# Kernel optimization log

Measured on AMD Instinct MI355X. Metric: run time of the kernel, lower is better.

## Reference

```python
import jax, jax.numpy as jnp
import numpy as np

N = 50000      # nodes
E = 800000     # edges (before self-loops)
F_IN = 256
H = 8          # heads layer 1
C = 64         # hidden channels per head
OUT = 40       # classes
NEG_SLOPE = 0.2


def setup_inputs() -> dict:
    key = jax.random.key(0)
    ks = jax.random.split(key, 10)
    sc = 0.05
    return {
        "x": jax.random.normal(ks[0], (N, F_IN), jnp.float32),
        "edge_index": jax.random.randint(ks[1], (2, E), 0, N, dtype=jnp.int64),
        "W1": jax.random.normal(ks[2], (F_IN, H * C), jnp.float32) * sc,
        "a_src1": jax.random.normal(ks[3], (H, C), jnp.float32) * sc,
        "a_dst1": jax.random.normal(ks[4], (H, C), jnp.float32) * sc,
        "b1": jnp.zeros((H * C,), jnp.float32),
        "W2": jax.random.normal(ks[5], (H * C, OUT), jnp.float32) * sc,
        "a_src2": jax.random.normal(ks[6], (1, OUT), jnp.float32) * sc,
        "a_dst2": jax.random.normal(ks[7], (1, OUT), jnp.float32) * sc,
        "b2": jnp.zeros((OUT,), jnp.float32),
    }


def gat_layer(h_in, src, dst, W, a_s, a_d, b, heads, ch, concat, n):
    # h: [n, heads, ch] per-head linear transform
    h = (h_in @ W).reshape(n, heads, ch)
    alpha_s = jnp.sum(h * a_s, axis=-1)   # [n, heads]
    alpha_d = jnp.sum(h * a_d, axis=-1)   # [n, heads]
    # edge-wise raw attention logits [E, heads]
    e = jax.nn.leaky_relu(alpha_s[src] + alpha_d[dst], NEG_SLOPE)
    # segment softmax over incoming edges of each dst node
    m = jax.ops.segment_max(e, dst, num_segments=n)
    w = jnp.exp(e - m[dst])
    s = jax.ops.segment_sum(w, dst, num_segments=n)
    alpha = w / s[dst]                    # [E, heads]
    # scatter-aggregate messages: [n, heads, ch]
    out = jax.ops.segment_sum(h[src] * alpha[:, :, None], dst, num_segments=n)
    out = out.reshape(n, heads * ch) if concat else out.mean(axis=1)
    return out + b


def reference(x, edge_index, W1, a_src1, a_dst1, b1, W2, a_src2, a_dst2, b2):
    # add self-loops (PyG GATConv default); guarantees every dst has >=1 edge
    loop = jnp.arange(N, dtype=edge_index.dtype)
    src = jnp.concatenate([edge_index[0], loop])
    dst = jnp.concatenate([edge_index[1], loop])
    h = gat_layer(x, src, dst, W1, a_src1, a_dst1, b1, H, C, True, N)
    h = jax.nn.relu(h)  # dropout is identity in eval mode
    out = gat_layer(h, src, dst, W2, a_src2, a_dst2, b2, 1, OUT, False, N)
    return jax.nn.log_softmax(out, axis=1)
```

## Files before the change

kernel.cpp:

```cpp
#include <hip/hip_runtime.h>

#define N_NODES 50000
#define N_EDGES 800000
#define F_INK   256
#define HC      512
#define OUT_C   40
#define OUT_P   48
#define NEG     0.2f
#define CAP     64
#define GEMM_NB 782

typedef short short8 __attribute__((ext_vector_type(8)));
typedef float f32x4 __attribute__((ext_vector_type(4)));
typedef float f32x2 __attribute__((ext_vector_type(2)));

__device__ __forceinline__ float bf2f(unsigned short u) {
    union { unsigned int i; float f; } v; v.i = ((unsigned int)u) << 16; return v.f;
}
__device__ __forceinline__ unsigned short f2bf(float f) {
    union { float f; unsigned int i; } v; v.f = f;
    unsigned int x = v.i;
    return (unsigned short)((x + 0x7fffu + ((x >> 16) & 1u)) >> 16);
}
__device__ __forceinline__ float bflo(unsigned int u) {
    union { unsigned int i; float f; } v; v.i = u << 16; return v.f;
}
__device__ __forceinline__ float bfhi(unsigned int u) {
    union { unsigned int i; float f; } v; v.i = u & 0xffff0000u; return v.f;
}
__device__ __forceinline__ bool ei_is64(const int* ei) {
    return ei[1] == 0 && ei[3] == 0 && ei[5] == 0;
}
__device__ __forceinline__ float lrelu(float x) { return x > 0.f ? x : NEG * x; }
__device__ __forceinline__ unsigned char f2fp8(float v) {
    return (unsigned char)(__builtin_amdgcn_cvt_pk_fp8_f32(v, v, 0, false) & 0xff);
}
__device__ __forceinline__ float fp82f(unsigned char b) {
    f32x2 p = __builtin_amdgcn_cvt_pk_f32_fp8((int)b, false);
    return p[0];
}

__global__ __launch_bounds__(256) void prep_k(const float* __restrict__ W1, const float* __restrict__ W2,
                       const float* __restrict__ s1, const float* __restrict__ d1, const float* __restrict__ b1,
                       const float* __restrict__ s2, const float* __restrict__ d2, const float* __restrict__ b2,
                       unsigned short* __restrict__ W1p, unsigned short* __restrict__ W2p,
                       unsigned short* __restrict__ s1c, unsigned short* __restrict__ d1c,
                       unsigned short* __restrict__ b1c, unsigned short* __restrict__ s2c,
                       unsigned short* __restrict__ d2c, unsigned short* __restrict__ b2c,
                       int* __restrict__ cnt, int* __restrict__ srcs) {
    int b = blockIdx.x;
    if (b < 512) {
        int t = b * 256 + threadIdx.x;
        int k = t / HC, n = t % HC;
        int s = k >> 5, q = (k >> 3) & 3, j = k & 7;
        W1p[((((s << 2) + q) * HC + n) << 3) + j] = f2bf(W1[k * HC + n]);
    } else if (b < 608) {
        int t = (b - 512) * 256 + threadIdx.x;
        int k = t / OUT_P, n = t % OUT_P;
        int s = k >> 5, q = (k >> 3) & 3, j = k & 7;
        unsigned short v = (n < OUT_C) ? f2bf(W2[k * OUT_C + n]) : (unsigned short)0;
        W2p[((((s << 2) + q) * OUT_P + n) << 3) + j] = v;
    } else if (b == 608) {
        int t = threadIdx.x;
        for (int j = t; j < 512; j += 256) {
            s1c[j] = f2bf(s1[j]); d1c[j] = f2bf(d1[j]); b1c[j] = f2bf(b1[j]);
        }
        if (t < OUT_C) { s2c[t] = f2bf(s2[t]); d2c[t] = f2bf(d2[t]); b2c[t] = f2bf(b2[t]); }
    } else {
        int i = (b - 609) * 256 + threadIdx.x;
        if (i < N_NODES) {
            cnt[i] = 1;
            srcs[(size_t)i * CAP] = i;
        }
    }
}

__global__ __launch_bounds__(256) void gemm1_k(const float* __restrict__ x,
                                               const unsigned short* __restrict__ Wp,
                                               const unsigned short* __restrict__ a_s,
                                               const unsigned short* __restrict__ a_d,
                                               unsigned char* __restrict__ h1f8,
                                               float* __restrict__ as1, float* __restrict__ ad1,
                                               const int* __restrict__ ei,
                                               int* __restrict__ cnt, int* __restrict__ srcs) {
    __shared__ unsigned short xs[64 * 264];
    int tid = threadIdx.x;
    if (blockIdx.x >= GEMM_NB) {
        int e = (blockIdx.x - GEMM_NB) * 256 + tid;
        if (e < N_EDGES) {
            bool is64 = ei_is64(ei);
            int src = is64 ? ei[2 * e] : ei[e];
            int dst = is64 ? ei[2 * N_EDGES + 2 * e] : ei[N_EDGES + e];
            int pos = atomicAdd(&cnt[dst], 1);
            if (pos < CAP) srcs[(size_t)dst * CAP + pos] = src;
        }
        return;
    }
    int bm = blockIdx.x;
    int row0 = bm * 64;
#pragma unroll
    for (int it = 0; it < 16; it++) {
        int j = tid + it * 256;
        int r = j >> 6;
        int c = (j & 63) << 2;
        int rr = row0 + r; rr = rr < N_NODES ? rr : N_NODES - 1;
        float4 f = *reinterpret_cast<const float4*>(x + (size_t)rr * F_INK + c);
        unsigned int lo = (unsigned int)f2bf(f.x) | ((unsigned int)f2bf(f.y) << 16);
        unsigned int hi = (unsigned int)f2bf(f.z) | ((unsigned int)f2bf(f.w) << 16);
        *reinterpret_cast<uint2*>(&xs[r * 264 + c]) = make_uint2(lo, hi);
    }
    __syncthreads();
    int w = tid >> 6, lane = tid & 63;
    int q = lane >> 4, l16 = lane & 15;
    short8 a[8];
#pragma unroll
    for (int s = 0; s < 8; s++)
        a[s] = *reinterpret_cast<const short8*>(&xs[(w * 16 + l16) * 264 + s * 32 + q * 8]);
    int orow = row0 + w * 16 + q * 4;
#pragma unroll
    for (int bn = 0; bn < 8; bn++) {
        f32x4 acc[4];
#pragma unroll
        for (int t = 0; t < 4; t++) acc[t] = (f32x4){0.f, 0.f, 0.f, 0.f};
#pragma unroll
        for (int s = 0; s < 8; s++) {
#pragma unroll
            for (int t = 0; t < 4; t++) {
                int col = bn * 64 + t * 16 + l16;
                short8 b = *reinterpret_cast<const short8*>(Wp + ((((s << 2) + q) * HC + col) << 3));
                acc[t] = __builtin_amdgcn_mfma_f32_16x16x32_bf16(a[s], b, acc[t], 0, 0, 0);
            }
        }
        float sa0 = 0.f, sa1 = 0.f, sa2 = 0.f, sa3 = 0.f;
        float da0 = 0.f, da1 = 0.f, da2 = 0.f, da3 = 0.f;
#pragma unroll
        for (int t = 0; t < 4; t++) {
            int col = bn * 64 + t * 16 + l16;
            float asc = bf2f(a_s[col]);
            float adc = bf2f(a_d[col]);
            float v0 = acc[t][0], v1 = acc[t][1], v2 = acc[t][2], v3 = acc[t][3];
            sa0 += v0 * asc; da0 += v0 * adc;
            sa1 += v1 * asc; da1 += v1 * adc;
            sa2 += v2 * asc; da2 += v2 * adc;
            sa3 += v3 * asc; da3 += v3 * adc;
            if (orow + 3 < N_NODES) {
                h1f8[(size_t)(orow + 0) * HC + col] = f2fp8(v0);
                h1f8[(size_t)(orow + 1) * HC + col] = f2fp8(v1);
                h1f8[(size_t)(orow + 2) * HC + col] = f2fp8(v2);
                h1f8[(size_t)(orow + 3) * HC + col] = f2fp8(v3);
            } else {
                if (orow + 0 < N_NODES) h1f8[(size_t)(orow + 0) * HC + col] = f2fp8(v0);
                if (orow + 1 < N_NODES) h1f8[(size_t)(orow + 1) * HC + col] = f2fp8(v1);
                if (orow + 2 < N_NODES) h1f8[(size_t)(orow + 2) * HC + col] = f2fp8(v2);
                if (orow + 3 < N_NODES) h1f8[(size_t)(orow + 3) * HC + col] = f2fp8(v3);
            }
        }
#pragma unroll
        for (int m = 1; m < 16; m <<= 1) {
            sa0 += __shfl_xor(sa0, m, 64); sa1 += __shfl_xor(sa1, m, 64);
            sa2 += __shfl_xor(sa2, m, 64); sa3 += __shfl_xor(sa3, m, 64);
            da0 += __shfl_xor(da0, m, 64); da1 += __shfl_xor(da1, m, 64);
            da2 += __shfl_xor(da2, m, 64); da3 += __shfl_xor(da3, m, 64);
        }
        if (l16 < 4) {
            int rr = orow + l16;
            float sav = (l16 == 0) ? sa0 : (l16 == 1) ? sa1 : (l16 == 2) ? sa2 : sa3;
            float dav = (l16 == 0) ? da0 : (l16 == 1) ? da1 : (l16 == 2) ? da2 : da3;
            if (rr < N_NODES) { as1[rr * 8 + bn] = sav; ad1[rr * 8 + bn] = dav; }
        }
    }
}

#define ACCPK(u, wgt)                                                        \
    {                                                                        \
        f32x2 p0 = __builtin_amdgcn_cvt_pk_f32_fp8((int)(u).x, false);       \
        f32x2 p1 = __builtin_amdgcn_cvt_pk_f32_fp8((int)(u).x, true);        \
        f32x2 p2 = __builtin_amdgcn_cvt_pk_f32_fp8((int)(u).y, false);       \
        f32x2 p3 = __builtin_amdgcn_cvt_pk_f32_fp8((int)(u).y, true);        \
        f32x2 wv = {(wgt), (wgt)};                                           \
        acc01 += wv * p0; acc23 += wv * p1;                                  \
        acc45 += wv * p2; acc67 += wv * p3;                                  \
    }

__global__ __launch_bounds__(256) void agg1_k(const unsigned char* __restrict__ h1f8,
                                              const float* __restrict__ as1,
                                              const float* __restrict__ ad1,
                                              const int* __restrict__ cnt,
                                              const int* __restrict__ srcs,
                                              const unsigned short* __restrict__ b1,
                                              const unsigned short* __restrict__ W2p,
                                              const unsigned short* __restrict__ a_s2,
                                              const unsigned short* __restrict__ a_d2,
                                              unsigned char* __restrict__ h2f8,
                                              float* __restrict__ as2, float* __restrict__ ad2) {
    __shared__ unsigned short rows[16 * 520];
    __shared__ float sAs[16], sAd[16];
    __shared__ int ctr;
    int tid = threadIdx.x;
    if (tid < 16) { sAs[tid] = 0.f; sAd[tid] = 0.f; }
    if (tid == 0) ctr = 0;
    __syncthreads();
    int w = tid >> 6, lane = tid & 63;
    int h = lane >> 3;
    int base = blockIdx.x * 16;
    uint4 ub = *(reinterpret_cast<const uint4*>(b1) + lane);
    for (;;) {
        int rl = 0;
        if (lane == 0) rl = atomicAdd(&ctr, 1);
        rl = __shfl(rl, 0, 64);
        if (rl >= 16) break;
        int wid = base + rl;
        float adv = ad1[wid * 8 + h];
        f32x2 acc01 = {0.f, 0.f}, acc23 = {0.f, 0.f}, acc45 = {0.f, 0.f}, acc67 = {0.f, 0.f};
        float sumw = 0.f;
        int e = wid * CAP, e1 = e + cnt[wid];
        for (; e + 12 <= e1; e += 12) {
            int s[12];
            float A[12];
            uint2 u[12];
#pragma unroll
            for (int j = 0; j < 12; j++) s[j] = srcs[e + j];
#pragma unroll
            for (int j = 0; j < 12; j++) A[j] = as1[s[j] * 8 + h];
#pragma unroll
            for (int j = 0; j < 12; j++)
                u[j] = reinterpret_cast<const uint2*>(h1f8 + (size_t)s[j] * HC)[lane];
#pragma unroll
            for (int j = 0; j < 12; j++) {
                float wj = __expf(lrelu(A[j] + adv));
                sumw += wj;
                ACCPK(u[j], wj)
            }
        }
        for (; e + 4 <= e1; e += 4) {
            int s[4];
            float A[4];
            uint2 u[4];
#pragma unroll
            for (int j = 0; j < 4; j++) s[j] = srcs[e + j];
#pragma unroll
            for (int j = 0; j < 4; j++) A[j] = as1[s[j] * 8 + h];
#pragma unroll
            for (int j = 0; j < 4; j++)
                u[j] = reinterpret_cast<const uint2*>(h1f8 + (size_t)s[j] * HC)[lane];
#pragma unroll
            for (int j = 0; j < 4; j++) {
                float wj = __expf(lrelu(A[j] + adv));
                sumw += wj;
                ACCPK(u[j], wj)
            }
        }
        for (; e < e1; e++) {
            int s0 = srcs[e];
            float wj = __expf(lrelu(as1[s0 * 8 + h] + adv));
            uint2 u0 = reinterpret_cast<const uint2*>(h1f8 + (size_t)s0 * HC)[lane];
            sumw += wj;
            ACCPK(u0, wj)
        }
        float inv = 1.f / sumw;
        float o0 = fmaxf(acc01[0] * inv + bflo(ub.x), 0.f);
        float o1 = fmaxf(acc01[1] * inv + bfhi(ub.x), 0.f);
        float o2 = fmaxf(acc23[0] * inv + bflo(ub.y), 0.f);
        float o3 = fmaxf(acc23[1] * inv + bfhi(ub.y), 0.f);
        float o4 = fmaxf(acc45[0] * inv + bflo(ub.z), 0.f);
        float o5 = fmaxf(acc45[1] * inv + bfhi(ub.z), 0.f);
        float o6 = fmaxf(acc67[0] * inv + bflo(ub.w), 0.f);
        float o7 = fmaxf(acc67[1] * inv + bfhi(ub.w), 0.f);
        uint4 r;
        r.x = (unsigned int)f2bf(o0) | ((unsigned int)f2bf(o1) << 16);
        r.y = (unsigned int)f2bf(o2) | ((unsigned int)f2bf(o3) << 16);
        r.z = (unsigned int)f2bf(o4) | ((unsigned int)f2bf(o5) << 16);
        r.w = (unsigned int)f2bf(o6) | ((unsigned int)f2bf(o7) << 16);
        *reinterpret_cast<uint4*>(&rows[rl * 520 + lane * 8]) = r;
    }
    __syncthreads();
    if (w < 3) {
        int q = lane >> 4, l16 = lane & 15;
        int col = w * 16 + l16;
        f32x4 acc = (f32x4){0.f, 0.f, 0.f, 0.f};
#pragma unroll
        for (int s = 0; s < HC / 32; s++) {
            short8 a = *reinterpret_cast<const short8*>(&rows[l16 * 520 + s * 32 + q * 8]);
            short8 b = *reinterpret_cast<const short8*>(W2p + ((((s << 2) + q) * OUT_P + col) << 3));
            acc = __builtin_amdgcn_mfma_f32_16x16x32_bf16(a, b, acc, 0, 0, 0);
        }
        float sa0 = 0.f, sa1 = 0.f, sa2 = 0.f, sa3 = 0.f;
        float da0 = 0.f, da1 = 0.f, da2 = 0.f, da3 = 0.f;
        if (col < OUT_C) {
            float asc = bf2f(a_s2[col]);
            float adc = bf2f(a_d2[col]);
            sa0 = acc[0] * asc; da0 = acc[0] * adc;
            sa1 = acc[1] * asc; da1 = acc[1] * adc;
            sa2 = acc[2] * asc; da2 = acc[2] * adc;
            sa3 = acc[3] * asc; da3 = acc[3] * adc;
#pragma unroll
            for (int r = 0; r < 4; r++)
                h2f8[(size_t)(base + q * 4 + r) * 64 + col] = f2fp8(acc[r]);
        }
#pragma unroll
        for (int m = 1; m < 16; m <<= 1) {
            sa0 += __shfl_xor(sa0, m, 64); sa1 += __shfl_xor(sa1, m, 64);
            sa2 += __shfl_xor(sa2, m, 64); sa3 += __shfl_xor(sa3, m, 64);
            da0 += __shfl_xor(da0, m, 64); da1 += __shfl_xor(da1, m, 64);
            da2 += __shfl_xor(da2, m, 64); da3 += __shfl_xor(da3, m, 64);
        }
        if (l16 < 4) {
            int rr = q * 4 + l16;
            float sav = (l16 == 0) ? sa0 : (l16 == 1) ? sa1 : (l16 == 2) ? sa2 : sa3;
            float dav = (l16 == 0) ? da0 : (l16 == 1) ? da1 : (l16 == 2) ? da2 : da3;
            atomicAdd(&sAs[rr], sav);
            atomicAdd(&sAd[rr], dav);
        }
    }
    __syncthreads();
    if (tid < 16) {
        as2[base + tid] = sAs[tid];
        ad2[base + tid] = sAd[tid];
    }
}

__global__ __launch_bounds__(256) void agg2_k(const unsigned char* __restrict__ h2f8,
                                              const float* __restrict__ as2,
                                              const float* __restrict__ ad2,
                                              const int* __restrict__ cnt,
                                              const int* __restrict__ srcs,
                                              const unsigned short* __restrict__ b2,
                                              float* __restrict__ outp) {
    int wid = blockIdx.x * 4 + (threadIdx.x >> 6);
    if (wid >= N_NODES) return;
    int lane = threadIdx.x & 63;
    bool act = lane < OUT_C;
    int lclamp = act ? lane : 0;
    float adv = ad2[wid];
    float acc = 0.f, sumw = 0.f;
    int e = wid * CAP, e1 = e + cnt[wid];
    for (; e + 4 <= e1; e += 4) {
        int s0 = srcs[e], s1 = srcs[e + 1], s2 = srcs[e + 2], s3 = srcs[e + 3];
        float A0 = as2[s0], A1 = as2[s1], A2 = as2[s2], A3 = as2[s3];
        unsigned char c0 = h2f8[(size_t)s0 * 64 + lclamp];
        unsigned char c1 = h2f8[(size_t)s1 * 64 + lclamp];
        unsigned char c2 = h2f8[(size_t)s2 * 64 + lclamp];
        unsigned char c3 = h2f8[(size_t)s3 * 64 + lclamp];
        float w0 = __expf(lrelu(A0 + adv));
        float w1 = __expf(lrelu(A1 + adv));
        float w2 = __expf(lrelu(A2 + adv));
        float w3 = __expf(lrelu(A3 + adv));
        sumw += (w0 + w1) + (w2 + w3);
        acc += w0 * fp82f(c0) + w1 * fp82f(c1) + w2 * fp82f(c2) + w3 * fp82f(c3);
    }
    for (; e < e1; e++) {
        int s0 = srcs[e];
        float w0 = __expf(lrelu(as2[s0] + adv));
        sumw += w0;
        acc += w0 * fp82f(h2f8[(size_t)s0 * 64 + lclamp]);
    }
    float o = acc / sumw + bf2f(b2[lclamp]);
    float mval = act ? o : -1e30f;
#pragma unroll
    for (int m = 32; m >= 1; m >>= 1) mval = fmaxf(mval, __shfl_xor(mval, m, 64));
    float ex = act ? __expf(o - mval) : 0.f;
#pragma unroll
    for (int m = 32; m >= 1; m >>= 1) ex += __shfl_xor(ex, m, 64);
    float res = o - mval - __logf(ex);
    if (act) outp[(size_t)wid * OUT_C + lane] = res;
}

extern "C" void kernel_launch(void* const* d_in, const int* in_sizes, int n_in,
                              void* d_out, int out_size, void* d_ws, size_t ws_size,
                              hipStream_t stream) {
    const float* x      = (const float*)d_in[0];
    const int*   ei     = (const int*)d_in[1];
    const float* W1     = (const float*)d_in[2];
    const float* as1raw = (const float*)d_in[3];
    const float* ad1raw = (const float*)d_in[4];
    const float* b1raw  = (const float*)d_in[5];
    const float* W2     = (const float*)d_in[6];
    const float* as2raw = (const float*)d_in[7];
    const float* ad2raw = (const float*)d_in[8];
    const float* b2raw  = (const float*)d_in[9];
    float* out = (float*)d_out;

    char* p = (char*)d_ws;
    auto alloc = [&](size_t bytes) -> char* {
        char* r = p;
        p += (bytes + 255) & ~(size_t)255;
        return r;
    };
    unsigned short* s1c  = (unsigned short*)alloc(512 * 2);
    unsigned short* d1c  = (unsigned short*)alloc(512 * 2);
    unsigned short* b1c  = (unsigned short*)alloc(512 * 2);
    unsigned short* s2c  = (unsigned short*)alloc(OUT_C * 2);
    unsigned short* d2c  = (unsigned short*)alloc(OUT_C * 2);
    unsigned short* b2c  = (unsigned short*)alloc(OUT_C * 2);
    unsigned char*  h1f8 = (unsigned char*)alloc((size_t)N_NODES * HC);
    unsigned char*  h2f8 = (unsigned char*)alloc((size_t)N_NODES * 64);
    float* as1  = (float*)alloc((size_t)N_NODES * 8 * 4);
    float* ad1  = (float*)alloc((size_t)N_NODES * 8 * 4);
    float* as2  = (float*)alloc((size_t)N_NODES * 4);
    float* ad2  = (float*)alloc((size_t)N_NODES * 4);
    int* cnt    = (int*)alloc((size_t)N_NODES * 4);
    int* srcs   = (int*)alloc((size_t)N_NODES * CAP * 4);
    unsigned short* W1p = (unsigned short*)alloc((size_t)F_INK * HC * 2);
    unsigned short* W2p = (unsigned short*)alloc((size_t)HC * OUT_P * 2);
    (void)ws_size; (void)in_sizes; (void)n_in; (void)out_size;

    const int NB = (N_NODES + 255) / 256;
    const int SCAT_NB = (N_EDGES + 255) / 256;

    prep_k<<<609 + NB, 256, 0, stream>>>(W1, W2, as1raw, ad1raw, b1raw, as2raw, ad2raw, b2raw,
                                         W1p, W2p, s1c, d1c, b1c, s2c, d2c, b2c, cnt, srcs);
    gemm1_k<<<GEMM_NB + SCAT_NB, 256, 0, stream>>>(x, W1p, s1c, d1c, h1f8, as1, ad1,
                                                   ei, cnt, srcs);
    agg1_k<<<N_NODES / 16, 256, 0, stream>>>(h1f8, as1, ad1, cnt, srcs, b1c,
                                             W2p, s2c, d2c, h2f8, as2, ad2);
    agg2_k<<<(N_NODES + 3) / 4, 256, 0, stream>>>(h2f8, as2, ad2, cnt, srcs, b2c, out);
}
```

Before: 279.0 us.

## Partition edge scatter by destination range, pad counters, pack layer-2 scores into rows

```diff
diff --git a/kernel.cpp b/kernel.cpp
--- a/kernel.cpp
+++ b/kernel.cpp
@@ -9,6 +9,9 @@
 #define NEG     0.2f
 #define CAP     64
 #define GEMM_NB 782
+#define CHUNKS  782
+#define PART_SZ 6250
+#define SCAT_NB (CHUNKS * 8)
 
 typedef short short8 __attribute__((ext_vector_type(8)));
 typedef float f32x4 __attribute__((ext_vector_type(4)));
@@ -47,7 +50,7 @@
                        unsigned short* __restrict__ s1c, unsigned short* __restrict__ d1c,
                        unsigned short* __restrict__ b1c, unsigned short* __restrict__ s2c,
                        unsigned short* __restrict__ d2c, unsigned short* __restrict__ b2c,
-                       int* __restrict__ cnt, int* __restrict__ srcs) {
+                       int* __restrict__ cnt) {
     int b = blockIdx.x;
     if (b < 512) {
         int t = b * 256 + threadIdx.x;
@@ -68,10 +71,7 @@
         if (t < OUT_C) { s2c[t] = f2bf(s2[t]); d2c[t] = f2bf(d2[t]); b2c[t] = f2bf(b2[t]); }
     } else {
         int i = (b - 609) * 256 + threadIdx.x;
-        if (i < N_NODES) {
-            cnt[i] = 1;
-            srcs[(size_t)i * CAP] = i;
-        }
+        if (i < N_NODES) cnt[i * 16] = 0;
     }
 }
 
@@ -86,13 +86,46 @@
     __shared__ unsigned short xs[64 * 264];
     int tid = threadIdx.x;
     if (blockIdx.x >= GEMM_NB) {
-        int e = (blockIdx.x - GEMM_NB) * 256 + tid;
-        if (e < N_EDGES) {
-            bool is64 = ei_is64(ei);
-            int src = is64 ? ei[2 * e] : ei[e];
-            int dst = is64 ? ei[2 * N_EDGES + 2 * e] : ei[N_EDGES + e];
-            int pos = atomicAdd(&cnt[dst], 1);
-            if (pos < CAP) srcs[(size_t)dst * CAP + pos] = src;
+        int sb = blockIdx.x - GEMM_NB;
+        int part = blockIdx.x & 7;
+        int chunk = sb >> 3;
+        int lo = part * PART_SZ;
+        bool is64 = ei_is64(ei);
+        int e0 = chunk * 1024 + (tid << 2);
+        int s[4], d[4];
+        bool vld[4];
+        if (chunk < CHUNKS - 1) {
+            if (is64) {
+                int4 a0 = *reinterpret_cast<const int4*>(ei + 2 * e0);
+                int4 a1 = *reinterpret_cast<const int4*>(ei + 2 * e0 + 4);
+                int4 c0 = *reinterpret_cast<const int4*>(ei + 2 * N_EDGES + 2 * e0);
+                int4 c1 = *reinterpret_cast<const int4*>(ei + 2 * N_EDGES + 2 * e0 + 4);
+                s[0] = a0.x; s[1] = a0.z; s[2] = a1.x; s[3] = a1.z;
+                d[0] = c0.x; d[1] = c0.z; d[2] = c1.x; d[3] = c1.z;
+            } else {
+                int4 a0 = *reinterpret_cast<const int4*>(ei + e0);
+                int4 c0 = *reinterpret_cast<const int4*>(ei + N_EDGES + e0);
+                s[0] = a0.x; s[1] = a0.y; s[2] = a0.z; s[3] = a0.w;
+                d[0] = c0.x; d[1] = c0.y; d[2] = c0.z; d[3] = c0.w;
+            }
+            vld[0] = vld[1] = vld[2] = vld[3] = true;
+        } else {
+#pragma unroll
+            for (int j = 0; j < 4; j++) {
+                int e = e0 + j;
+                vld[j] = e < N_EDGES;
+                int ec = vld[j] ? e : 0;
+                s[j] = is64 ? ei[2 * ec] : ei[ec];
+                d[j] = is64 ? ei[2 * N_EDGES + 2 * ec] : ei[N_EDGES + ec];
+            }
+        }
+#pragma unroll
+        for (int j = 0; j < 4; j++) {
+            int dj = d[j];
+            if (vld[j] && dj >= lo && dj < lo + PART_SZ) {
+                int pos = atomicAdd(&cnt[dj * 16], 1);
+                if (pos < CAP) srcs[(size_t)dj * CAP + pos] = s[j];
+            }
         }
         return;
     }
@@ -191,8 +224,7 @@
                                               const unsigned short* __restrict__ W2p,
                                               const unsigned short* __restrict__ a_s2,
                                               const unsigned short* __restrict__ a_d2,
-                                              unsigned char* __restrict__ h2f8,
-                                              float* __restrict__ as2, float* __restrict__ ad2) {
+                                              unsigned char* __restrict__ h2f8) {
     __shared__ unsigned short rows[16 * 520];
     __shared__ float sAs[16], sAd[16];
     __shared__ int ctr;
@@ -213,7 +245,7 @@
         float adv = ad1[wid * 8 + h];
         f32x2 acc01 = {0.f, 0.f}, acc23 = {0.f, 0.f}, acc45 = {0.f, 0.f}, acc67 = {0.f, 0.f};
         float sumw = 0.f;
-        int e = wid * CAP, e1 = e + cnt[wid];
+        int e = wid * CAP, e1 = e + cnt[wid * 16];
         for (; e + 12 <= e1; e += 12) {
             int s[12];
             float A[12];
@@ -254,6 +286,12 @@
             int s0 = srcs[e];
             float wj = __expf(lrelu(as1[s0 * 8 + h] + adv));
             uint2 u0 = reinterpret_cast<const uint2*>(h1f8 + (size_t)s0 * HC)[lane];
+            sumw += wj;
+            ACCPK(u0, wj)
+        }
+        {
+            float wj = __expf(lrelu(as1[wid * 8 + h] + adv));
+            uint2 u0 = reinterpret_cast<const uint2*>(h1f8 + (size_t)wid * HC)[lane];
             sumw += wj;
             ACCPK(u0, wj)
         }
@@ -314,14 +352,13 @@
     }
     __syncthreads();
     if (tid < 16) {
-        as2[base + tid] = sAs[tid];
-        ad2[base + tid] = sAd[tid];
+        unsigned char* r = h2f8 + (size_t)(base + tid) * 64;
+        *reinterpret_cast<float*>(r + 40) = sAs[tid];
+        *reinterpret_cast<float*>(r + 44) = sAd[tid];
     }
 }
 
 __global__ __launch_bounds__(256) void agg2_k(const unsigned char* __restrict__ h2f8,
-                                              const float* __restrict__ as2,
-                                              const float* __restrict__ ad2,
                                               const int* __restrict__ cnt,
                                               const int* __restrict__ srcs,
                                               const unsigned short* __restrict__ b2,
@@ -331,16 +368,29 @@
     int lane = threadIdx.x & 63;
     bool act = lane < OUT_C;
     int lclamp = act ? lane : 0;
-    float adv = ad2[wid];
-    float acc = 0.f, sumw = 0.f;
-    int e = wid * CAP, e1 = e + cnt[wid];
+    const unsigned char* rd = h2f8 + (size_t)wid * 64;
+    float adv = *reinterpret_cast<const float*>(rd + 44);
+    float acc, sumw;
+    {
+        float w0 = __expf(lrelu(*reinterpret_cast<const float*>(rd + 40) + adv));
+        sumw = w0;
+        acc = w0 * fp82f(rd[lclamp]);
+    }
+    int e = wid * CAP, e1 = e + cnt[wid * 16];
     for (; e + 4 <= e1; e += 4) {
         int s0 = srcs[e], s1 = srcs[e + 1], s2 = srcs[e + 2], s3 = srcs[e + 3];
-        float A0 = as2[s0], A1 = as2[s1], A2 = as2[s2], A3 = as2[s3];
-        unsigned char c0 = h2f8[(size_t)s0 * 64 + lclamp];
-        unsigned char c1 = h2f8[(size_t)s1 * 64 + lclamp];
-        unsigned char c2 = h2f8[(size_t)s2 * 64 + lclamp];
-        unsigned char c3 = h2f8[(size_t)s3 * 64 + lclamp];
+        const unsigned char* r0 = h2f8 + (size_t)s0 * 64;
+        const unsigned char* r1 = h2f8 + (size_t)s1 * 64;
+        const unsigned char* r2 = h2f8 + (size_t)s2 * 64;
+        const unsigned char* r3 = h2f8 + (size_t)s3 * 64;
+        float A0 = *reinterpret_cast<const float*>(r0 + 40);
+        float A1 = *reinterpret_cast<const float*>(r1 + 40);
+        float A2 = *reinterpret_cast<const float*>(r2 + 40);
+        float A3 = *reinterpret_cast<const float*>(r3 + 40);
+        unsigned char c0 = r0[lclamp];
+        unsigned char c1 = r1[lclamp];
+        unsigned char c2 = r2[lclamp];
+        unsigned char c3 = r3[lclamp];
         float w0 = __expf(lrelu(A0 + adv));
         float w1 = __expf(lrelu(A1 + adv));
         float w2 = __expf(lrelu(A2 + adv));
@@ -350,9 +400,10 @@
     }
     for (; e < e1; e++) {
         int s0 = srcs[e];
-        float w0 = __expf(lrelu(as2[s0] + adv));
+        const unsigned char* r0 = h2f8 + (size_t)s0 * 64;
+        float w0 = __expf(lrelu(*reinterpret_cast<const float*>(r0 + 40) + adv));
         sumw += w0;
-        acc += w0 * fp82f(h2f8[(size_t)s0 * 64 + lclamp]);
+        acc += w0 * fp82f(r0[lclamp]);
     }
     float o = acc / sumw + bf2f(b2[lclamp]);
     float mval = act ? o : -1e30f;
@@ -396,22 +447,19 @@
     unsigned char*  h2f8 = (unsigned char*)alloc((size_t)N_NODES * 64);
     float* as1  = (float*)alloc((size_t)N_NODES * 8 * 4);
     float* ad1  = (float*)alloc((size_t)N_NODES * 8 * 4);
-    float* as2  = (float*)alloc((size_t)N_NODES * 4);
-    float* ad2  = (float*)alloc((size_t)N_NODES * 4);
-    int* cnt    = (int*)alloc((size_t)N_NODES * 4);
+    int* cnt    = (int*)alloc((size_t)N_NODES * 64);
     int* srcs   = (int*)alloc((size_t)N_NODES * CAP * 4);
     unsigned short* W1p = (unsigned short*)alloc((size_t)F_INK * HC * 2);
     unsigned short* W2p = (unsigned short*)alloc((size_t)HC * OUT_P * 2);
     (void)ws_size; (void)in_sizes; (void)n_in; (void)out_size;
 
     const int NB = (N_NODES + 255) / 256;
-    const int SCAT_NB = (N_EDGES + 255) / 256;
 
     prep_k<<<609 + NB, 256, 0, stream>>>(W1, W2, as1raw, ad1raw, b1raw, as2raw, ad2raw, b2raw,
-                                         W1p, W2p, s1c, d1c, b1c, s2c, d2c, b2c, cnt, srcs);
+                                         W1p, W2p, s1c, d1c, b1c, s2c, d2c, b2c, cnt);
     gemm1_k<<<GEMM_NB + SCAT_NB, 256, 0, stream>>>(x, W1p, s1c, d1c, h1f8, as1, ad1,
                                                    ei, cnt, srcs);
     agg1_k<<<N_NODES / 16, 256, 0, stream>>>(h1f8, as1, ad1, cnt, srcs, b1c,
-                                             W2p, s2c, d2c, h2f8, as2, ad2);
-    agg2_k<<<(N_NODES + 3) / 4, 256, 0, stream>>>(h2f8, as2, ad2, cnt, srcs, b2c, out);
-}
+                                             W2p, s2c, d2c, h2f8);
+    agg2_k<<<(N_NODES + 3) / 4, 256, 0, stream>>>(h2f8, cnt, srcs, b2c, out);
+}
```

New measurement: 288.9 us. 3.6% more time.
